# Kernel tuning notes

Hardware: AMD Instinct MI355X
Metric: run time of the kernel (lower is better)

Reference implementation:

```python
import jax, jax.numpy as jnp
import numpy as np

B, L, D = 4, 2048, 1024
H, DK, DV = 16, 64, 64
EPS = 1e-6


def setup_inputs() -> dict:
    key = jax.random.key(0)
    ks = jax.random.split(key, 8)
    s = 0.02
    return {
        "q": jax.random.normal(ks[0], (B, L, D), dtype=jnp.float32),
        "k": jax.random.normal(ks[1], (B, L, D), dtype=jnp.float32),
        "v": jax.random.normal(ks[2], (B, L, D), dtype=jnp.float32),
        "Wq": jax.random.normal(ks[3], (H * DK, D), dtype=jnp.float32) * s,
        "Wk": jax.random.normal(ks[4], (H * DK, D), dtype=jnp.float32) * s,
        "Wv": jax.random.normal(ks[5], (H * DV, D), dtype=jnp.float32) * s,
        "Wfc": jax.random.normal(ks[6], (D, H * DV), dtype=jnp.float32) * s,
        "ln_g": jnp.ones((D,), dtype=jnp.float32),
        "ln_b": jnp.zeros((D,), dtype=jnp.float32),
    }


def reference(q, k, v, Wq, Wk, Wv, Wfc, ln_g, ln_b):
    residual = q
    # projections (Linear: x @ W.T), reshape to [B, H, L, d]
    qh = (q @ Wq.T).reshape(B, L, H, DK).transpose(0, 2, 1, 3)
    kh = (k @ Wk.T).reshape(B, L, H, DK).transpose(0, 2, 1, 3)
    vh = (v @ Wv.T).reshape(B, L, H, DV).transpose(0, 2, 1, 3)
    temperature = jnp.float32(DK) ** 0.5
    # scores [B, H, Lq, Lk]
    scores = jnp.einsum("bhqd,bhkd->bhqk", qh / temperature, kh)
    attn = jax.nn.softmax(scores, axis=-1)
    ctx = jnp.einsum("bhqk,bhkd->bhqd", attn, vh)  # [B, H, L, DV]
    ctx = ctx.transpose(0, 2, 1, 3).reshape(B, L, H * DV)
    out = ctx @ Wfc.T + residual
    # LayerNorm(eps=1e-6)
    mu = jnp.mean(out, axis=-1, keepdims=True)
    var = jnp.var(out, axis=-1, keepdims=True)
    out = (out - mu) * jax.lax.rsqrt(var + EPS) * ln_g + ln_b
    return out, attn
```

## Files before the change

kernel.cpp:

```cpp
#include <hip/hip_runtime.h>
#include <hip/hip_bf16.h>

typedef __bf16 bf16;
typedef __bf16 bf16x8 __attribute__((ext_vector_type(8)));
typedef __bf16 bf16x4 __attribute__((ext_vector_type(4)));
typedef __bf16 bf16x2 __attribute__((ext_vector_type(2)));
typedef float f32x4 __attribute__((ext_vector_type(4)));
typedef float f32x16 __attribute__((ext_vector_type(16)));
typedef unsigned int u32x4 __attribute__((ext_vector_type(4)));

#define MFMA_BF16(a, b, c) __builtin_amdgcn_mfma_f32_16x16x32_bf16((a), (b), (c), 0, 0, 0)
#define MFMA32(a, b, c) __builtin_amdgcn_mfma_f32_32x32x16_bf16((a), (b), (c), 0, 0, 0)

#if defined(__has_builtin)
#if __has_builtin(__builtin_amdgcn_exp2f)
#define EXP2F(x) __builtin_amdgcn_exp2f(x)
#endif
#endif
#ifndef EXP2F
#define EXP2F(x) exp2f(x)
#endif

static constexpr int Bc = 4, Lc = 2048, Dc = 1024, Hc = 16, DKc = 64;
static constexpr int BLc = Bc * Lc;
static constexpr float CEXP = 0.18033688011112042f;

__device__ inline unsigned pk2(float a, float b) {
  bf16x2 t;
  t[0] = (bf16)a;
  t[1] = (bf16)b;
  return __builtin_bit_cast(unsigned, t);
}

__global__ __launch_bounds__(256) void cvt_all(const float* __restrict__ s0,
                                               const float* __restrict__ s1,
                                               const float* __restrict__ s2,
                                               const float* __restrict__ s3,
                                               bf16* __restrict__ dst) {
  size_t i = ((size_t)blockIdx.x * 256 + threadIdx.x) * 8;
  const float* srcs[4] = {s0, s1, s2, s3};
  const float* sp = srcs[i >> 20] + (i & 1048575);
  float4 f0 = ((const float4*)sp)[0];
  float4 f1 = ((const float4*)sp)[1];
  bf16x8 o;
  o[0] = (bf16)f0.x; o[1] = (bf16)f0.y; o[2] = (bf16)f0.z; o[3] = (bf16)f0.w;
  o[4] = (bf16)f1.x; o[5] = (bf16)f1.y; o[6] = (bf16)f1.z; o[7] = (bf16)f1.w;
  *(bf16x8*)(dst + i) = o;
}

__global__ __launch_bounds__(256) void qkv_gemm(const float* __restrict__ qin,
                                                const float* __restrict__ kin,
                                                const float* __restrict__ vin,
                                                const bf16* __restrict__ Wb,
                                                bf16* __restrict__ qh,
                                                bf16* __restrict__ kh,
                                                bf16* __restrict__ vt) {
  __shared__ bf16 As[128][72];
  __shared__ bf16 Bs[128][72];
  const int t = threadIdx.x;
  const int lane = t & 63, wid = t >> 6;
  const int wr = wid >> 1, wc = wid & 1;
  const int which = blockIdx.y >> 3;
  const int m0 = blockIdx.x * 128, n0 = (blockIdx.y & 7) * 128;
  const float* A = which == 0 ? qin : which == 1 ? kin : vin;
  const bf16* Bw = Wb + ((size_t)which << 20);
  const int sub = t & 7, srow = t >> 3;

  f32x4 acc[4][4] = {};

  for (int kt = 0; kt < 1024; kt += 64) {
#pragma unroll
    for (int s = 0; s < 4; ++s) {
      int r = srow + 32 * s;
      const float4* pa = (const float4*)(A + (size_t)(m0 + r) * 1024 + kt + sub * 8);
      float4 f0 = pa[0], f1 = pa[1];
      bf16x8 o;
      o[0] = (bf16)f0.x; o[1] = (bf16)f0.y; o[2] = (bf16)f0.z; o[3] = (bf16)f0.w;
      o[4] = (bf16)f1.x; o[5] = (bf16)f1.y; o[6] = (bf16)f1.z; o[7] = (bf16)f1.w;
      *(bf16x8*)&As[r][sub * 8] = o;
    }
#pragma unroll
    for (int s = 0; s < 4; ++s) {
      int r = srow + 32 * s;
      u32x4 u = *(const u32x4*)(Bw + (size_t)(n0 + r) * 1024 + kt + sub * 8);
      *(u32x4*)&Bs[r][sub * 8] = u;
    }
    __syncthreads();
#pragma unroll
    for (int c = 0; c < 2; ++c) {
      const int ko = c * 32 + (lane >> 4) * 8;
      bf16x8 af[4], bfr[4];
#pragma unroll
      for (int m = 0; m < 4; ++m)
        af[m] = *(const bf16x8*)&As[wr * 64 + m * 16 + (lane & 15)][ko];
#pragma unroll
      for (int n = 0; n < 4; ++n)
        bfr[n] = *(const bf16x8*)&Bs[wc * 64 + n * 16 + (lane & 15)][ko];
#pragma unroll
      for (int m = 0; m < 4; ++m)
#pragma unroll
        for (int n = 0; n < 4; ++n)
          acc[m][n] = MFMA_BF16(af[m], bfr[n], acc[m][n]);
    }
    __syncthreads();
  }

  const int rbase = m0 + wr * 64 + (lane >> 4) * 4;
  const int cbase = n0 + wc * 64 + (lane & 15);
  if (which < 2) {
    bf16* C = which == 0 ? qh : kh;
#pragma unroll
    for (int m = 0; m < 4; ++m)
#pragma unroll
      for (int n = 0; n < 4; ++n)
#pragma unroll
        for (int r = 0; r < 4; ++r) {
          size_t row = (size_t)(rbase + m * 16 + r);
          size_t col = (size_t)(cbase + n * 16);
          C[row * 1024 + col] = (bf16)acc[m][n][r];
        }
  } else {
#pragma unroll
    for (int m = 0; m < 4; ++m)
#pragma unroll
      for (int n = 0; n < 4; ++n) {
        int row = rbase + m * 16;
        int col = cbase + n * 16;
        bf16x4 o;
#pragma unroll
        for (int r = 0; r < 4; ++r) o[r] = (bf16)acc[m][n][r];
        size_t dst = ((size_t)((row >> 11) << 10) + col) * 2048 + (row & 2047);
        *(bf16x4*)(vt + dst) = o;
      }
  }
}

__global__ __launch_bounds__(256) void fc_gemm(const bf16* __restrict__ A,
                                               const bf16* __restrict__ Bw,
                                               float* __restrict__ C,
                                               const float* __restrict__ resid) {
  __shared__ bf16 As[128][72];
  __shared__ bf16 Bs[128][72];
  const int t = threadIdx.x;
  const int lane = t & 63, wid = t >> 6;
  const int wr = wid >> 1, wc = wid & 1;
  const int m0 = blockIdx.x * 128, n0 = blockIdx.y * 128;
  const int sub = t & 7, srow = t >> 3;

  f32x4 acc[4][4] = {};

  for (int kt = 0; kt < 1024; kt += 64) {
#pragma unroll
    for (int s = 0; s < 4; ++s) {
      int r = srow + 32 * s;
      u32x4 u = *(const u32x4*)(A + (size_t)(m0 + r) * 1024 + kt + sub * 8);
      *(u32x4*)&As[r][sub * 8] = u;
    }
#pragma unroll
    for (int s = 0; s < 4; ++s) {
      int r = srow + 32 * s;
      u32x4 u = *(const u32x4*)(Bw + (size_t)(n0 + r) * 1024 + kt + sub * 8);
      *(u32x4*)&Bs[r][sub * 8] = u;
    }
    __syncthreads();
#pragma unroll
    for (int c = 0; c < 2; ++c) {
      const int ko = c * 32 + (lane >> 4) * 8;
      bf16x8 af[4], bfr[4];
#pragma unroll
      for (int m = 0; m < 4; ++m)
        af[m] = *(const bf16x8*)&As[wr * 64 + m * 16 + (lane & 15)][ko];
#pragma unroll
      for (int n = 0; n < 4; ++n)
        bfr[n] = *(const bf16x8*)&Bs[wc * 64 + n * 16 + (lane & 15)][ko];
#pragma unroll
      for (int m = 0; m < 4; ++m)
#pragma unroll
        for (int n = 0; n < 4; ++n)
          acc[m][n] = MFMA_BF16(af[m], bfr[n], acc[m][n]);
    }
    __syncthreads();
  }

  const int rbase = m0 + wr * 64 + (lane >> 4) * 4;
  const int cbase = n0 + wc * 64 + (lane & 15);
#pragma unroll
  for (int m = 0; m < 4; ++m)
#pragma unroll
    for (int n = 0; n < 4; ++n)
#pragma unroll
      for (int r = 0; r < 4; ++r) {
        size_t row = (size_t)(rbase + m * 16 + r);
        size_t col = (size_t)(cbase + n * 16);
        C[row * 1024 + col] = acc[m][n][r] + resid[row * 1024 + col];
      }
}

__global__ __launch_bounds__(256, 4) void attn_kernel(const bf16* __restrict__ qh,
                                                      const bf16* __restrict__ kh,
                                                      const bf16* __restrict__ vt,
                                                      bf16* __restrict__ ctx,
                                                      float* __restrict__ attn_out) {
  __shared__ bf16 Ks[64][72];
  __shared__ bf16 Vs[64][72];
  const int t = threadIdx.x, lane = t & 63, w = t >> 6;
  const int hi = lane >> 5, ql = lane & 31;
  const int qt = blockIdx.x, h = blockIdx.y, b = blockIdx.z;
  const size_t rowbase = (size_t)b * 2048;
  const int qrow = qt * 128 + w * 32 + ql;
  const bf16* kbase = kh + rowbase * 1024 + h * 64;
  const bf16* vbase = vt + (size_t)(b * 16 + h) * 64 * 2048;
  const int sub = t & 7, srow = t >> 3;

  bf16x8 qf[4];
  {
    const bf16* qp = qh + (rowbase + qrow) * 1024 + h * 64 + hi * 8;
#pragma unroll
    for (int c = 0; c < 4; ++c) qf[c] = *(const bf16x8*)(qp + c * 16);
  }

  f32x16 cacc[2] = {};
  float zacc = 0.f;

  for (int kt = 0; kt < 2048; kt += 64) {
    __syncthreads();
#pragma unroll
    for (int s = 0; s < 2; ++s) {
      int r = srow + 32 * s;
      *(u32x4*)&Ks[r][sub * 8] =
          *(const u32x4*)(kbase + (size_t)(kt + r) * 1024 + sub * 8);
      *(u32x4*)&Vs[r][sub * 8] =
          *(const u32x4*)(vbase + (size_t)r * 2048 + kt + sub * 8);
    }
    __syncthreads();
#pragma unroll
    for (int sb = 0; sb < 2; ++sb) {
      f32x16 s = {};
#pragma unroll
      for (int c = 0; c < 4; ++c) {
        bf16x8 kf = *(const bf16x8*)&Ks[sb * 32 + ql][c * 16 + hi * 8];
        s = MFMA32(kf, qf[c], s);
      }
      unsigned pv[4][2];
#pragma unroll
      for (int o = 0; o < 4; ++o)
#pragma unroll
        for (int d = 0; d < 2; ++d) {
          float e0 = EXP2F(s[o * 4 + 2 * d] * CEXP);
          float e1 = EXP2F(s[o * 4 + 2 * d + 1] * CEXP);
          zacc += e0 + e1;
          pv[o][d] = pk2(e0, e1);
        }
      bf16x8 pa[2];
#pragma unroll
      for (int c = 0; c < 2; ++c) {
        u32x4 pu;
#pragma unroll
        for (int d = 0; d < 2; ++d) {
          unsigned a = pv[2 * c][d], bq = pv[2 * c + 1][d];
          unsigned as = (unsigned)__shfl_xor((int)a, 32);
          unsigned bs = (unsigned)__shfl_xor((int)bq, 32);
          pu[d] = hi ? bs : a;
          pu[2 + d] = hi ? bq : as;
        }
        pa[c] = __builtin_bit_cast(bf16x8, pu);
      }
#pragma unroll
      for (int n = 0; n < 2; ++n)
#pragma unroll
        for (int c = 0; c < 2; ++c) {
          bf16x8 vf = *(const bf16x8*)&Vs[n * 32 + ql][sb * 32 + c * 16 + hi * 8];
          cacc[n] = MFMA32(pa[c], vf, cacc[n]);
        }
    }
  }

  float z = zacc + __shfl_xor(zacc, 32);
  float rz = 1.0f / z;

#pragma unroll
  for (int g = 0; g < 16; ++g) {
    int crow = (g & 3) + 8 * (g >> 2) + 4 * hi;
    float rv = __shfl(rz, crow);
    size_t row = rowbase + (size_t)(qt * 128 + w * 32 + crow);
    ctx[row * 1024 + h * 64 + ql] = (bf16)(cacc[0][g] * rv);
    ctx[row * 1024 + h * 64 + 32 + ql] = (bf16)(cacc[1][g] * rv);
  }

  float* abase = attn_out + ((size_t)(b * 16 + h) * 2048 + qrow) * 2048;
  for (int kt = 0; kt < 2048; kt += 128) {
    __syncthreads();
#pragma unroll
    for (int s = 0; s < 2; ++s) {
      int r = srow + 32 * s;
      *(u32x4*)&Ks[r][sub * 8] =
          *(const u32x4*)(kbase + (size_t)(kt + r) * 1024 + sub * 8);
      *(u32x4*)&Vs[r][sub * 8] =
          *(const u32x4*)(kbase + (size_t)(kt + 64 + r) * 1024 + sub * 8);
    }
    __syncthreads();
#pragma unroll
    for (int half = 0; half < 2; ++half) {
      const bf16(*Kb)[72] = half ? Vs : Ks;
      const int koff = kt + half * 64;
#pragma unroll
      for (int sb = 0; sb < 2; ++sb) {
        f32x16 s = {};
#pragma unroll
        for (int c = 0; c < 4; ++c) {
          bf16x8 kf = *(const bf16x8*)&Kb[sb * 32 + ql][c * 16 + hi * 8];
          s = MFMA32(kf, qf[c], s);
        }
#pragma unroll
        for (int o = 0; o < 4; ++o) {
          float4 v4;
          v4.x = EXP2F(s[o * 4 + 0] * CEXP) * rz;
          v4.y = EXP2F(s[o * 4 + 1] * CEXP) * rz;
          v4.z = EXP2F(s[o * 4 + 2] * CEXP) * rz;
          v4.w = EXP2F(s[o * 4 + 3] * CEXP) * rz;
          *(float4*)(abase + koff + sb * 32 + o * 8 + hi * 4) = v4;
        }
      }
    }
  }
}

__global__ __launch_bounds__(256) void ln_kernel(float* __restrict__ io,
                                                 const float* __restrict__ g,
                                                 const float* __restrict__ bta) {
  const int row = blockIdx.x, t = threadIdx.x;
  float4* rp = (float4*)(io + (size_t)row * 1024);
  float4 v = rp[t];
  float s = v.x + v.y + v.z + v.w;
  float s2 = v.x * v.x + v.y * v.y + v.z * v.z + v.w * v.w;
#pragma unroll
  for (int off = 32; off >= 1; off >>= 1) {
    s += __shfl_xor(s, off);
    s2 += __shfl_xor(s2, off);
  }
  __shared__ float ls[4], ls2[4];
  const int w = t >> 6;
  if ((t & 63) == 0) { ls[w] = s; ls2[w] = s2; }
  __syncthreads();
  s = ls[0] + ls[1] + ls[2] + ls[3];
  s2 = ls2[0] + ls2[1] + ls2[2] + ls2[3];
  float mu = s * (1.f / 1024.f);
  float var = s2 * (1.f / 1024.f) - mu * mu;
  float rs = rsqrtf(var + 1e-6f);
  float4 gv = ((const float4*)g)[t];
  float4 bv = ((const float4*)bta)[t];
  v.x = (v.x - mu) * rs * gv.x + bv.x;
  v.y = (v.y - mu) * rs * gv.y + bv.y;
  v.z = (v.z - mu) * rs * gv.z + bv.z;
  v.w = (v.w - mu) * rs * gv.w + bv.w;
  rp[t] = v;
}

extern "C" void kernel_launch(void* const* d_in, const int* in_sizes, int n_in,
                              void* d_out, int out_size, void* d_ws, size_t ws_size,
                              hipStream_t stream) {
  (void)in_sizes; (void)n_in; (void)out_size; (void)ws_size;
  const float* q    = (const float*)d_in[0];
  const float* k    = (const float*)d_in[1];
  const float* v    = (const float*)d_in[2];
  const float* Wq   = (const float*)d_in[3];
  const float* Wk   = (const float*)d_in[4];
  const float* Wv   = (const float*)d_in[5];
  const float* Wfc  = (const float*)d_in[6];
  const float* ln_g = (const float*)d_in[7];
  const float* ln_b = (const float*)d_in[8];

  char* ws = (char*)d_ws;
  const size_t MB = 1024ull * 1024ull;
  bf16* wall = (bf16*)(ws + 0 * MB);
  bf16* wfcb = (bf16*)(ws + 6 * MB);
  bf16* qh   = (bf16*)(ws + 8 * MB);
  bf16* kh   = (bf16*)(ws + 24 * MB);
  bf16* vt   = (bf16*)(ws + 40 * MB);
  bf16* ctx  = (bf16*)(ws + 56 * MB);

  float* outp  = (float*)d_out;
  float* attnp = outp + (size_t)BLc * Dc;

  cvt_all<<<2048, 256, 0, stream>>>(Wq, Wk, Wv, Wfc, wall);

  qkv_gemm<<<dim3(64, 24), 256, 0, stream>>>(q, k, v, wall, qh, kh, vt);

  attn_kernel<<<dim3(16, 16, 4), 256, 0, stream>>>(qh, kh, vt, ctx, attnp);

  fc_gemm<<<dim3(64, 8), 256, 0, stream>>>(ctx, wfcb, outp, q);
  ln_kernel<<<8192, 256, 0, stream>>>(outp, ln_g, ln_b);
}
```

Before: 476.9 us.

## Compute softmax denominator first, then fuse attn write with PV pass

Reorders the attention kernel into a cheap QK-only pass that accumulates the softmax denominator, followed by a single pass that computes normalized probabilities, writes the attn matrix, and does the PV MFMA. The old structure did a QK+PV pass and then a third QK pass just to write attn. The number of QK passes is unchanged, but the PV work now sits alongside the large attn stores, which may overlap memory writes with compute. The ctx output no longer needs the per-row rescale shuffle. Probabilities are normalized before the bf16 pack, which changes rounding slightly.

```diff
diff --git a/kernel.cpp b/kernel.cpp
--- a/kernel.cpp
+++ b/kernel.cpp
@@ -219,9 +219,39 @@
     for (int c = 0; c < 4; ++c) qf[c] = *(const bf16x8*)(qp + c * 16);
   }
 
+  float zacc = 0.f;
+  for (int kt = 0; kt < 2048; kt += 128) {
+    __syncthreads();
+#pragma unroll
+    for (int s = 0; s < 2; ++s) {
+      int r = srow + 32 * s;
+      *(u32x4*)&Ks[r][sub * 8] =
+          *(const u32x4*)(kbase + (size_t)(kt + r) * 1024 + sub * 8);
+      *(u32x4*)&Vs[r][sub * 8] =
+          *(const u32x4*)(kbase + (size_t)(kt + 64 + r) * 1024 + sub * 8);
+    }
+    __syncthreads();
+#pragma unroll
+    for (int half = 0; half < 2; ++half) {
+      const bf16(*Kb)[72] = half ? Vs : Ks;
+#pragma unroll
+      for (int sb = 0; sb < 2; ++sb) {
+        f32x16 s = {};
+#pragma unroll
+        for (int c = 0; c < 4; ++c) {
+          bf16x8 kf = *(const bf16x8*)&Kb[sb * 32 + ql][c * 16 + hi * 8];
+          s = MFMA32(kf, qf[c], s);
+        }
+#pragma unroll
+        for (int j = 0; j < 16; ++j) zacc += EXP2F(s[j] * CEXP);
+      }
+    }
+  }
+  const float z = zacc + __shfl_xor(zacc, 32);
+  const float rz = 1.0f / z;
+
   f32x16 cacc[2] = {};
-  float zacc = 0.f;
-
+  float* abase = attn_out + ((size_t)(b * 16 + h) * 2048 + qrow) * 2048;
   for (int kt = 0; kt < 2048; kt += 64) {
     __syncthreads();
 #pragma unroll
@@ -243,14 +273,17 @@
       }
       unsigned pv[4][2];
 #pragma unroll
-      for (int o = 0; o < 4; ++o)
-#pragma unroll
-        for (int d = 0; d < 2; ++d) {
-          float e0 = EXP2F(s[o * 4 + 2 * d] * CEXP);
-          float e1 = EXP2F(s[o * 4 + 2 * d + 1] * CEXP);
-          zacc += e0 + e1;
-          pv[o][d] = pk2(e0, e1);
-        }
+      for (int o = 0; o < 4; ++o) {
+        float e0 = EXP2F(s[o * 4 + 0] * CEXP) * rz;
+        float e1 = EXP2F(s[o * 4 + 1] * CEXP) * rz;
+        float e2 = EXP2F(s[o * 4 + 2] * CEXP) * rz;
+        float e3 = EXP2F(s[o * 4 + 3] * CEXP) * rz;
+        float4 v4;
+        v4.x = e0; v4.y = e1; v4.z = e2; v4.w = e3;
+        *(float4*)(abase + kt + sb * 32 + o * 8 + hi * 4) = v4;
+        pv[o][0] = pk2(e0, e1);
+        pv[o][1] = pk2(e2, e3);
+      }
       bf16x8 pa[2];
 #pragma unroll
       for (int c = 0; c < 2; ++c) {
@@ -275,53 +308,12 @@
     }
   }
 
-  float z = zacc + __shfl_xor(zacc, 32);
-  float rz = 1.0f / z;
-
 #pragma unroll
   for (int g = 0; g < 16; ++g) {
     int crow = (g & 3) + 8 * (g >> 2) + 4 * hi;
-    float rv = __shfl(rz, crow);
     size_t row = rowbase + (size_t)(qt * 128 + w * 32 + crow);
-    ctx[row * 1024 + h * 64 + ql] = (bf16)(cacc[0][g] * rv);
-    ctx[row * 1024 + h * 64 + 32 + ql] = (bf16)(cacc[1][g] * rv);
-  }
-
-  float* abase = attn_out + ((size_t)(b * 16 + h) * 2048 + qrow) * 2048;
-  for (int kt = 0; kt < 2048; kt += 128) {
-    __syncthreads();
-#pragma unroll
-    for (int s = 0; s < 2; ++s) {
-      int r = srow + 32 * s;
-      *(u32x4*)&Ks[r][sub * 8] =
-          *(const u32x4*)(kbase + (size_t)(kt + r) * 1024 + sub * 8);
-      *(u32x4*)&Vs[r][sub * 8] =
-          *(const u32x4*)(kbase + (size_t)(kt + 64 + r) * 1024 + sub * 8);
-    }
-    __syncthreads();
-#pragma unroll
-    for (int half = 0; half < 2; ++half) {
-      const bf16(*Kb)[72] = half ? Vs : Ks;
-      const int koff = kt + half * 64;
-#pragma unroll
-      for (int sb = 0; sb < 2; ++sb) {
-        f32x16 s = {};
-#pragma unroll
-        for (int c = 0; c < 4; ++c) {
-          bf16x8 kf = *(const bf16x8*)&Kb[sb * 32 + ql][c * 16 + hi * 8];
-          s = MFMA32(kf, qf[c], s);
-        }
-#pragma unroll
-        for (int o = 0; o < 4; ++o) {
-          float4 v4;
-          v4.x = EXP2F(s[o * 4 + 0] * CEXP) * rz;
-          v4.y = EXP2F(s[o * 4 + 1] * CEXP) * rz;
-          v4.z = EXP2F(s[o * 4 + 2] * CEXP) * rz;
-          v4.w = EXP2F(s[o * 4 + 3] * CEXP) * rz;
-          *(float4*)(abase + koff + sb * 32 + o * 8 + hi * 4) = v4;
-        }
-      }
-    }
+    ctx[row * 1024 + h * 64 + ql] = (bf16)cacc[0][g];
+    ctx[row * 1024 + h * 64 + 32 + ql] = (bf16)cacc[1][g];
   }
 }
 
```

Measured after the change: 527.7 us. +10.7%, slower.
